# Performance work log

Hardware: AMD Instinct MI355X
Metric: run time of the kernel (lower is better)

The kernel has to match this reference:

```python
import jax, jax.numpy as jnp
import numpy as np

DIM = 1024
HEADS = 8
EV = DIM  # dim*expand - dim with expand=2
P = 2.0   # power-softmax exponent
EPS = 1e-5


def setup_inputs() -> dict:
    key = jax.random.key(0)
    k1, k2, k3 = jax.random.split(key, 3)
    B, L = 4, 2048
    x = jax.random.normal(k1, (B, L, DIM), dtype=jnp.float32)
    gamma = jnp.ones((DIM,), dtype=jnp.float32)
    beta = jnp.zeros((DIM,), dtype=jnp.float32)
    # torch nn.Linear weights are [out_features, in_features]
    w_qkv = jax.random.normal(k2, (5 * DIM, DIM), dtype=jnp.float32) * (DIM ** -0.5)
    w_out = jax.random.normal(k3, (DIM, 2 * DIM), dtype=jnp.float32) * ((2 * DIM) ** -0.5)
    return {"x": x, "gamma": gamma, "beta": beta, "w_qkv": w_qkv, "w_out": w_out}


def _layernorm(x, gamma, beta):
    xf = x.astype(jnp.float32)
    mu = jnp.mean(xf, axis=-1, keepdims=True)
    var = jnp.mean(jnp.square(xf - mu), axis=-1, keepdims=True)
    return ((xf - mu) * jax.lax.rsqrt(var + EPS)) * gamma + beta


def _p_softmax(scores, scale, p):
    # scores: [B,H,L,L] with -inf on masked entries
    s = scores.astype(jnp.float32) * scale
    if p == 1.0:
        return jax.nn.softmax(s, axis=-1)
    lse = jax.nn.logsumexp(s * p, axis=-1, keepdims=True) / p
    return jnp.exp(s - lse)


def _attention(q, k, v, heads, p):
    B, L, D = q.shape
    hd = D // heads
    q = q.reshape(B, L, heads, hd).transpose(0, 2, 1, 3)  # bhld
    k = k.reshape(B, L, heads, hd).transpose(0, 2, 1, 3)
    v = v.reshape(B, L, heads, hd).transpose(0, 2, 1, 3)
    scores = jnp.einsum('bhqd,bhkd->bhqk', q, k)
    mask = jnp.tril(jnp.ones((L, L), dtype=bool))
    scores = jnp.where(mask, scores, -jnp.inf)
    probs = _p_softmax(scores, hd ** -0.5, p).astype(q.dtype)
    out = jnp.einsum('bhqk,bhkd->bhqd', probs, v)
    return out.transpose(0, 2, 1, 3).reshape(B, L, D)


def reference(x, gamma, beta, w_qkv, w_out):
    h = _layernorm(x, gamma, beta).astype(x.dtype)
    proj = h @ w_qkv.T  # [B,L,5*DIM]
    q, k, v, lin, pre = jnp.split(proj, np.cumsum([DIM, DIM, DIM, EV]), axis=-1)
    attn = _attention(q, k, v, HEADS, P)
    branch = jnp.concatenate([lin * jax.nn.gelu(pre, approximate=False), attn], axis=-1)
    return x + branch @ w_out.T
```

## Files before the change

kernel.cpp:

```cpp
#include <hip/hip_runtime.h>
#include <hip/hip_bf16.h>
#include <math.h>

#define DIMD 1024
#define LSEQ 2048
#define BATCH 4
#define NHEAD 8
#define HD 128
#define NROWS (BATCH*LSEQ)
#define PROJC (5*DIMD)
#define BRC (2*DIMD)

typedef __attribute__((ext_vector_type(8))) short short8;
typedef __attribute__((ext_vector_type(4))) short short4v;
typedef __attribute__((ext_vector_type(4))) float floatx4;

__device__ __forceinline__ float bf2f(short s) {
  unsigned int u = ((unsigned int)(unsigned short)s) << 16;
  return __builtin_bit_cast(float, u);
}
__device__ __forceinline__ short f2bf(float f) {
  unsigned int u = __builtin_bit_cast(unsigned int, f);
  unsigned int lsb = (u >> 16) & 1u;
  u += 0x7fffu + lsb;
  return (short)(u >> 16);
}

__device__ __forceinline__ void gl2lds16(const short* g, short* l) {
  __builtin_amdgcn_global_load_lds(
      (const __attribute__((address_space(1))) unsigned int*)(unsigned long long)g,
      (__attribute__((address_space(3))) unsigned int*)(unsigned int)(unsigned long long)l,
      16, 0, 0);
}

__device__ __forceinline__ void wgbar() {
  asm volatile("" ::: "memory");
  __builtin_amdgcn_s_barrier();
  asm volatile("" ::: "memory");
}

__global__ __launch_bounds__(256) void cvt2_kernel(const float* __restrict__ s1,
    short* __restrict__ d1, int n1_4, const float* __restrict__ s2,
    short* __restrict__ d2, int n2_4) {
  int i = blockIdx.x * 256 + threadIdx.x;
  const float* src; short* dst;
  if (i < n1_4) { src = s1; dst = d1; }
  else { i -= n1_4; if (i >= n2_4) return; src = s2; dst = d2; }
  float4 v = *(const float4*)(src + (size_t)i * 4);
  short4v o;
  o[0] = f2bf(v.x); o[1] = f2bf(v.y); o[2] = f2bf(v.z); o[3] = f2bf(v.w);
  *(short4v*)(dst + (size_t)i * 4) = o;
}

__global__ __launch_bounds__(256) void ln_kernel(const float* __restrict__ x,
    const float* __restrict__ gamma, const float* __restrict__ beta,
    short* __restrict__ h) {
  int row = blockIdx.x;
  int c = threadIdx.x * 4;
  const float* xr = x + (size_t)row * DIMD;
  float4 v = *(const float4*)(xr + c);
  float f[4] = {v.x, v.y, v.z, v.w};
  float sum = 0.f, sq = 0.f;
  for (int i = 0; i < 4; ++i) { sum += f[i]; sq += f[i]*f[i]; }
  for (int off = 1; off < 64; off <<= 1) {
    sum += __shfl_xor(sum, off);
    sq  += __shfl_xor(sq, off);
  }
  __shared__ float red[8];
  int wid = threadIdx.x >> 6;
  if ((threadIdx.x & 63) == 0) { red[wid*2] = sum; red[wid*2+1] = sq; }
  __syncthreads();
  sum = red[0]+red[2]+red[4]+red[6];
  sq  = red[1]+red[3]+red[5]+red[7];
  float mu = sum * (1.0f/DIMD);
  float var = sq * (1.0f/DIMD) - mu*mu;
  float rstd = rsqrtf(var + 1e-5f);
  float4 g = *(const float4*)(gamma + c);
  float4 bb = *(const float4*)(beta + c);
  float gg[4] = {g.x, g.y, g.z, g.w};
  float bv[4] = {bb.x, bb.y, bb.z, bb.w};
  short4v o;
  for (int i = 0; i < 4; ++i)
    o[i] = f2bf((f[i] - mu) * rstd * gg[i] + bv[i]);
  *(short4v*)(h + (size_t)row * DIMD + c) = o;
}


__device__ __forceinline__ void rd_a(const short* base, int s0, int s1,
                                     short8 (&a)[4][2]) {
#pragma unroll
  for (int m = 0; m < 4; ++m) {
    a[m][0] = *(const short8*)(base + m*16*64 + s0);
    a[m][1] = *(const short8*)(base + m*16*64 + s1);
  }
}
__device__ __forceinline__ void rd_b(const short* base, int s0, int s1,
                                     short8 (&b)[2][2]) {
#pragma unroll
  for (int n = 0; n < 2; ++n) {
    b[n][0] = *(const short8*)(base + n*16*64 + s0);
    b[n][1] = *(const short8*)(base + n*16*64 + s1);
  }
}
template<int QM, int QN>
__device__ __forceinline__ void qmm(const short8 (&a)[4][2], const short8 (&b)[2][2],
                                    floatx4 (&acc)[8][4]) {
  __builtin_amdgcn_s_setprio(1);
#pragma unroll
  for (int m = 0; m < 4; ++m)
#pragma unroll
    for (int n = 0; n < 2; ++n) {
      floatx4 c = acc[QM*4+m][QN*2+n];
      c = __builtin_amdgcn_mfma_f32_16x16x32_bf16(a[m][0], b[n][0], c, 0, 0, 0);
      c = __builtin_amdgcn_mfma_f32_16x16x32_bf16(a[m][1], b[n][1], c, 0, 0, 0);
      acc[QM*4+m][QN*2+n] = c;
    }
  __builtin_amdgcn_s_setprio(0);
}
__device__ __forceinline__ void stg2(const short* p, int K, short* lds) {
  gl2lds16(p, lds);
  gl2lds16(p + (size_t)64*K, lds + 64*64);
}
__device__ __forceinline__ void stg4(const short* p, int K, short* lds, int koff) {
  stg2(p + koff, K, lds);
  stg2(p + (size_t)128*K + koff, K, lds + 128*64);
}

__global__ __launch_bounds__(512, 2) void gemm256(const short* __restrict__ A,
    const short* __restrict__ W, short* __restrict__ C, int M, int N, int K) {
  __shared__ __align__(16) short AsF[2*256*64];
  __shared__ __align__(16) short WsF[2*256*64];
  const int tid = threadIdx.x;
  const int lane = tid & 63, wv = tid >> 6;
  const int wm = wv >> 2, wn = wv & 3;
  const int quad = lane >> 4, l16 = lane & 15;

  const int nbx = N >> 8;
  int cpx = gridDim.x >> 3;
  int orig = blockIdx.x;
  int wg = (orig & 7) * cpx + (orig >> 3);
  int bx = wg % nbx, by = wg / nbx;
  const int row0 = by << 8, col0 = bx << 8;

  const int lrow = lane >> 3;
  const int sslot = (lane & 7) ^ lrow;
  const short* pA = A + (size_t)(row0 + wv*8 + lrow) * K + sslot*8;
  const short* pW = W + (size_t)(col0 + wv*8 + lrow) * K + sslot*8;
  short* stA = AsF + wv*8*64;
  short* stW = WsF + wv*8*64;
  const short* aB = AsF + (wm*128 + l16)*64;
  const short* wB = WsF + (wn*64 + l16)*64;
  const int s0 = (quad ^ (l16 & 7)) << 3;
  const int s1 = s0 ^ 32;

  floatx4 acc[8][4] = {};
  short8 a[4][2], b0[2][2], b1[2][2];

  const int nktm = (K >> 6) - 1;

  stg4(pA, K, stA, 0);
  stg4(pW, K, stW, 0);
  stg4(pA, K, stA + 16384, 64);
  asm volatile("s_waitcnt vmcnt(4)" ::: "memory");
  wgbar();

  const int NT = K >> 6;
  for (int t = 0; t < NT; ++t) {
    const int cur = (t & 1) << 14;
    const int nxt = cur ^ 16384;
    const int kw1 = ((t + 1) & nktm) << 6;
    const int ka2 = ((t + 2) & nktm) << 6;
    rd_a(aB + cur, s0, s1, a);
    rd_b(wB + cur, s0, s1, b0);
    stg4(pW, K, stW + nxt, kw1);
    wgbar();
    qmm<0,0>(a, b0, acc);
    rd_b(wB + cur + 32*64, s0, s1, b1);
    wgbar();
    qmm<0,1>(a, b1, acc);
    rd_a(aB + cur + 64*64, s0, s1, a);
    wgbar();
    qmm<1,1>(a, b1, acc);
    wgbar();
    stg4(pA, K, stA + cur, ka2);
    qmm<1,0>(a, b0, acc);
    asm volatile("s_waitcnt vmcnt(4)" ::: "memory");
    wgbar();
  }
  asm volatile("s_waitcnt vmcnt(0)" ::: "memory");

#pragma unroll
  for (int i = 0; i < 8; ++i) {
    int r0 = row0 + wm*128 + i*16 + quad*4;
#pragma unroll
    for (int j = 0; j < 4; ++j) {
      int cc = col0 + wn*64 + j*16 + l16;
#pragma unroll
      for (int r = 0; r < 4; ++r)
        C[(size_t)(r0 + r) * N + cc] = f2bf(acc[i][j][r]);
    }
  }
}

template<int MODE>
__global__ __launch_bounds__(256) void gemm_bt(const short* __restrict__ A,
    const short* __restrict__ W, const float* __restrict__ X,
    void* __restrict__ Cv, int M, int N, int K) {
  __shared__ __align__(16) short As[128*64];
  __shared__ __align__(16) short Ws[128*64];
  int tid = threadIdx.x;
  int row0 = blockIdx.y * 128;
  int col0 = blockIdx.x * 128;
  int lane = tid & 63, wv = tid >> 6;
  int wr = (wv >> 1) * 64, wc = (wv & 1) * 64;
  int quad = lane >> 4, l16 = lane & 15;
  floatx4 acc[4][4] = {};
  int srow = lane >> 3;
  int gq = ((lane & 7) - srow) & 7;
  const short* Ag = A + (size_t)(row0 + wv*8 + srow) * K + gq*8;
  const short* Wg = W + (size_t)(col0 + wv*8 + srow) * K + gq*8;
  short* Al = As + wv*8*64;
  short* Wl = Ws + wv*8*64;
  int qsr0 = (((quad)     + (l16 & 7)) & 7) * 8;
  int qsr1 = (((quad + 4) + (l16 & 7)) & 7) * 8;
  for (int k0 = 0; k0 < K; k0 += 64) {
    __syncthreads();
    for (int c = 0; c < 4; ++c) {
      gl2lds16(Ag + k0 + (size_t)(c*32)*K, Al + c*32*64);
      gl2lds16(Wg + k0 + (size_t)(c*32)*K, Wl + c*32*64);
    }
    __syncthreads();
    short8 af[4], wf[4];
    for (int i = 0; i < 4; ++i) af[i] = *(const short8*)&As[(wr + i*16 + l16)*64 + qsr0];
    for (int j = 0; j < 4; ++j) wf[j] = *(const short8*)&Ws[(wc + j*16 + l16)*64 + qsr0];
    for (int i = 0; i < 4; ++i)
      for (int j = 0; j < 4; ++j)
        acc[i][j] = __builtin_amdgcn_mfma_f32_16x16x32_bf16(af[i], wf[j], acc[i][j], 0, 0, 0);
    for (int i = 0; i < 4; ++i) af[i] = *(const short8*)&As[(wr + i*16 + l16)*64 + qsr1];
    for (int j = 0; j < 4; ++j) wf[j] = *(const short8*)&Ws[(wc + j*16 + l16)*64 + qsr1];
    for (int i = 0; i < 4; ++i)
      for (int j = 0; j < 4; ++j)
        acc[i][j] = __builtin_amdgcn_mfma_f32_16x16x32_bf16(af[i], wf[j], acc[i][j], 0, 0, 0);
  }
  for (int i = 0; i < 4; ++i) {
    int r0 = row0 + wr + i*16 + quad*4;
    for (int j = 0; j < 4; ++j) {
      int cc = col0 + wc + j*16 + l16;
      for (int r = 0; r < 4; ++r) {
        float v = acc[i][j][r];
        size_t idx = (size_t)(r0 + r) * N + cc;
        if (MODE == 0) {
          ((short*)Cv)[idx] = f2bf(v);
        } else {
          ((float*)Cv)[idx] = v + X[idx];
        }
      }
    }
  }
}

__global__ __launch_bounds__(256) void gelu_kernel(const short* __restrict__ proj,
    short* __restrict__ branch) {
  int row = blockIdx.x;
  int c = threadIdx.x * 4;
  const short* pr = proj + (size_t)row * PROJC;
  short4v lin = *(const short4v*)(pr + 3*DIMD + c);
  short4v pre = *(const short4v*)(pr + 4*DIMD + c);
  short4v o;
  for (int i = 0; i < 4; ++i) {
    float xx = bf2f(pre[i]);
    float g = 0.5f * xx * (1.f + erff(xx * 0.70710678118654752f));
    o[i] = f2bf(bf2f(lin[i]) * g);
  }
  *(short4v*)(branch + (size_t)row * BRC + c) = o;
}

__global__ __launch_bounds__(256) void vt_kernel(const short* __restrict__ proj,
    short* __restrict__ vt) {
  int bh = blockIdx.y;
  int b = bh >> 3, hh = bh & 7;
  int l0 = blockIdx.x * 64;
  __shared__ short Ls[64][136];
  int tid = threadIdx.x;
  int r = tid >> 4, c = (tid & 15) * 8;
  const short* Vp = proj + (size_t)b * LSEQ * PROJC + 2*DIMD + hh*HD;
  for (int p = 0; p < 4; ++p)
    *(short8*)&Ls[r + p*16][c] = *(const short8*)(Vp + (size_t)(l0 + r + p*16) * PROJC + c);
  __syncthreads();
  int d = tid >> 1, lh = (tid & 1) * 32;
  short* outp = vt + ((size_t)bh * HD + d) * LSEQ + l0 + lh;
  for (int g = 0; g < 4; ++g) {
    short8 o;
    for (int j = 0; j < 8; ++j) o[j] = Ls[lh + g*8 + j][d];
    *(short8*)(outp + g*8) = o;
  }
}

__global__ __launch_bounds__(512) void attn_kernel(const short* __restrict__ proj,
    const short* __restrict__ vt, short* __restrict__ branch) {
  int bh = blockIdx.y;
  int b = bh >> 3, hh = bh & 7;
  int gx = blockIdx.x;
  int gsel = (bh < 16) ? gx : (15 - gx);
  int tid = threadIdx.x;
  int wv = tid >> 6, lane = tid & 63, quad = lane >> 4, l16 = lane & 15;
  int qsel = 2*gsel + ((wv < 4) ? 0 : 1);
  int qw = qsel * 64 + (wv & 3) * 16;

  const short* Qp  = proj + (size_t)b * LSEQ * PROJC + hh*HD;
  const short* Kp  = Qp + DIMD;
  const short* VTp = vt + (size_t)bh * HD * LSEQ;

  __shared__ short Ks[64][136];
  __shared__ short Vs[128][76];
  __shared__ short Ps[8][16][44];

  short8 qf[4];
  {
    const short* qrow = Qp + (size_t)(qw + l16) * PROJC;
    for (int s = 0; s < 4; ++s) qf[s] = *(const short8*)(qrow + s*32 + quad*8);
  }
  float lsum[4] = {0.f, 0.f, 0.f, 0.f};
  floatx4 O[8] = {};

  const float scale = 0.08838834764831845f;
  int NT = 2*gsel + 2;
  int krow = tid >> 4;
  int kcol = (tid & 15) * 8;
  int vd = tid >> 2;
  int vk = (tid & 3) * 8;

  short8 kv0 = *(const short8*)(Kp + (size_t)(krow) * PROJC + kcol);
  short8 kv1 = *(const short8*)(Kp + (size_t)(32 + krow) * PROJC + kcol);
  short8 vv0 = *(const short8*)(VTp + (size_t)vd * LSEQ + vk);
  short8 vv1 = *(const short8*)(VTp + (size_t)vd * LSEQ + 32 + vk);

  for (int kt = 0; kt < NT; ++kt) {
    int kb64 = kt * 64;
    __syncthreads();
    *(short8*)&Ks[krow][kcol]      = kv0;
    *(short8*)&Ks[krow + 32][kcol] = kv1;
    *(short8*)&Vs[vd][vk]          = vv0;
    *(short8*)&Vs[vd][32 + vk]     = vv1;
    {
      int ktn = (kt + 1 < NT) ? (kt + 1) : kt;
      int kb64n = ktn * 64;
      kv0 = *(const short8*)(Kp + (size_t)(kb64n + krow) * PROJC + kcol);
      kv1 = *(const short8*)(Kp + (size_t)(kb64n + 32 + krow) * PROJC + kcol);
      vv0 = *(const short8*)(VTp + (size_t)vd * LSEQ + kb64n + vk);
      vv1 = *(const short8*)(VTp + (size_t)vd * LSEQ + kb64n + 32 + vk);
    }
    __syncthreads();
    for (int hf = 0; hf < 2; ++hf) {
      int kb = kb64 + hf*32;
      if (kb <= qw + 15) {
        floatx4 s0 = {0.f,0.f,0.f,0.f}, s1 = {0.f,0.f,0.f,0.f};
        for (int s = 0; s < 4; ++s) {
          short8 kf0 = *(const short8*)&Ks[hf*32 + l16][s*32 + quad*8];
          short8 kf1 = *(const short8*)&Ks[hf*32 + 16 + l16][s*32 + quad*8];
          s0 = __builtin_amdgcn_mfma_f32_16x16x32_bf16(qf[s], kf0, s0, 0, 0, 0);
          s1 = __builtin_amdgcn_mfma_f32_16x16x32_bf16(qf[s], kf1, s1, 0, 0, 0);
        }
        int c0 = kb + l16, c1 = kb + 16 + l16;
        for (int r = 0; r < 4; ++r) {
          int q = qw + quad*4 + r;
          float w0 = (c0 <= q) ? __expf(s0[r] * scale) : 0.f;
          float w1 = (c1 <= q) ? __expf(s1[r] * scale) : 0.f;
          lsum[r] += w0*w0 + w1*w1;
          Ps[wv][quad*4+r][l16]      = f2bf(w0);
          Ps[wv][quad*4+r][16 + l16] = f2bf(w1);
        }
        asm volatile("s_waitcnt lgkmcnt(0)" ::: "memory");
        short8 pf = *(const short8*)&Ps[wv][l16][quad*8];
        for (int t8 = 0; t8 < 8; ++t8) {
          short8 vf = *(const short8*)&Vs[t8*16 + l16][hf*32 + quad*8];
          O[t8] = __builtin_amdgcn_mfma_f32_16x16x32_bf16(pf, vf, O[t8], 0, 0, 0);
        }
      }
    }
  }
  for (int r = 0; r < 4; ++r) {
    float l = lsum[r];
    for (int off = 1; off < 16; off <<= 1) l += __shfl_xor(l, off);
    float inv = rsqrtf(l);
    int q = qw + quad*4 + r;
    short* orow = branch + ((size_t)(b*LSEQ + q)) * BRC + DIMD + hh*HD;
    for (int t8 = 0; t8 < 8; ++t8)
      orow[t8*16 + l16] = f2bf(O[t8][r] * inv);
  }
}

extern "C" void kernel_launch(void* const* d_in, const int* in_sizes, int n_in,
                              void* d_out, int out_size, void* d_ws, size_t ws_size,
                              hipStream_t stream) {
  const float* x     = (const float*)d_in[0];
  const float* gamma = (const float*)d_in[1];
  const float* beta  = (const float*)d_in[2];
  const float* w_qkv = (const float*)d_in[3];
  const float* w_out = (const float*)d_in[4];
  float* out = (float*)d_out;

  char* ws = (char*)d_ws;
  short* h      = (short*)ws;
  short* proj   = (short*)(ws + (size_t)16*1024*1024);
  short* branch = (short*)(ws + (size_t)96*1024*1024);
  short* wq     = (short*)(ws + (size_t)128*1024*1024);
  short* wo     = (short*)(ws + (size_t)138*1024*1024);
  short* vt     = h;

  int n1 = PROJC*DIMD/4, n2 = DIMD*BRC/4;
  cvt2_kernel<<<(n1 + n2 + 255)/256, 256, 0, stream>>>(w_qkv, wq, n1, w_out, wo, n2);
  ln_kernel<<<NROWS, 256, 0, stream>>>(x, gamma, beta, h);
  gemm256<<<dim3((NROWS/256)*(PROJC/256)), 512, 0, stream>>>(h, wq, proj,
                                                             NROWS, PROJC, DIMD);
  gelu_kernel<<<NROWS, 256, 0, stream>>>(proj, branch);
  vt_kernel<<<dim3(LSEQ/64, BATCH*NHEAD), 256, 0, stream>>>(proj, vt);
  attn_kernel<<<dim3(16, BATCH*NHEAD), 512, 0, stream>>>(proj, vt, branch);
  gemm_bt<1><<<dim3(DIMD/128, NROWS/128), 256, 0, stream>>>(branch, wo, x, out,
                                                            NROWS, DIMD, BRC);
}
```

Baseline: 350.9 us.

## Replace output GEMM with double-buffered 128x256 pipelined kernel and XCD-aware block remap

Replaces the simple single-buffered 128x128 output-projection GEMM with a 512-thread kernel that computes 128x256 tiles. It double-buffers A and W tiles in LDS, issues global-to-LDS loads for the next k-step while MFMAs run, and uses XOR-swizzled LDS slots. It also remaps block indices so neighbouring tiles land on the same XCD, which should improve L2 reuse. The aim is to hide load latency and cut barrier stalls in the final GEMM, at the cost of more LDS per block and a more complex schedule.

```diff
diff --git a/kernel.cpp b/kernel.cpp
--- a/kernel.cpp
+++ b/kernel.cpp
@@ -85,7 +85,6 @@
   *(short4v*)(h + (size_t)row * DIMD + c) = o;
 }
 
-
 __device__ __forceinline__ void rd_a(const short* base, int s0, int s1,
                                      short8 (&a)[4][2]) {
 #pragma unroll
@@ -114,6 +113,21 @@
       c = __builtin_amdgcn_mfma_f32_16x16x32_bf16(a[m][0], b[n][0], c, 0, 0, 0);
       c = __builtin_amdgcn_mfma_f32_16x16x32_bf16(a[m][1], b[n][1], c, 0, 0, 0);
       acc[QM*4+m][QN*2+n] = c;
+    }
+  __builtin_amdgcn_s_setprio(0);
+}
+template<int QN>
+__device__ __forceinline__ void qmm2(const short8 (&a)[4][2], const short8 (&b)[2][2],
+                                     floatx4 (&acc)[4][4]) {
+  __builtin_amdgcn_s_setprio(1);
+#pragma unroll
+  for (int m = 0; m < 4; ++m)
+#pragma unroll
+    for (int n = 0; n < 2; ++n) {
+      floatx4 c = acc[m][QN*2+n];
+      c = __builtin_amdgcn_mfma_f32_16x16x32_bf16(a[m][0], b[n][0], c, 0, 0, 0);
+      c = __builtin_amdgcn_mfma_f32_16x16x32_bf16(a[m][1], b[n][1], c, 0, 0, 0);
+      acc[m][QN*2+n] = c;
     }
   __builtin_amdgcn_s_setprio(0);
 }
@@ -202,58 +216,76 @@
   }
 }
 
-template<int MODE>
-__global__ __launch_bounds__(256) void gemm_bt(const short* __restrict__ A,
+__global__ __launch_bounds__(512, 2) void gemm2(const short* __restrict__ A,
     const short* __restrict__ W, const float* __restrict__ X,
-    void* __restrict__ Cv, int M, int N, int K) {
-  __shared__ __align__(16) short As[128*64];
-  __shared__ __align__(16) short Ws[128*64];
-  int tid = threadIdx.x;
-  int row0 = blockIdx.y * 128;
-  int col0 = blockIdx.x * 128;
-  int lane = tid & 63, wv = tid >> 6;
-  int wr = (wv >> 1) * 64, wc = (wv & 1) * 64;
-  int quad = lane >> 4, l16 = lane & 15;
+    float* __restrict__ out, int M, int N, int K) {
+  __shared__ __align__(16) short As2[2*128*64];
+  __shared__ __align__(16) short Ws2[2*256*64];
+  const int tid = threadIdx.x;
+  const int lane = tid & 63, wv = tid >> 6;
+  const int wm = wv >> 2, wn = wv & 3;
+  const int quad = lane >> 4, l16 = lane & 15;
+
+  const int nbx = N >> 8;
+  int cpx = gridDim.x >> 3;
+  int orig = blockIdx.x;
+  int wg = (orig & 7) * cpx + (orig >> 3);
+  int bx = wg % nbx, by = wg / nbx;
+  const int row0 = by << 7, col0 = bx << 8;
+
+  const int lrow = lane >> 3;
+  const int sslot = (lane & 7) ^ lrow;
+  const short* pA = A + (size_t)(row0 + wv*8 + lrow) * K + sslot*8;
+  const short* pW = W + (size_t)(col0 + wv*8 + lrow) * K + sslot*8;
+  short* stA = As2 + wv*8*64;
+  short* stW = Ws2 + wv*8*64;
+  const short* aB = As2 + (wm*64 + l16)*64;
+  const short* wB = Ws2 + (wn*64 + l16)*64;
+  const int s0 = (quad ^ (l16 & 7)) << 3;
+  const int s1 = s0 ^ 32;
+
   floatx4 acc[4][4] = {};
-  int srow = lane >> 3;
-  int gq = ((lane & 7) - srow) & 7;
-  const short* Ag = A + (size_t)(row0 + wv*8 + srow) * K + gq*8;
-  const short* Wg = W + (size_t)(col0 + wv*8 + srow) * K + gq*8;
-  short* Al = As + wv*8*64;
-  short* Wl = Ws + wv*8*64;
-  int qsr0 = (((quad)     + (l16 & 7)) & 7) * 8;
-  int qsr1 = (((quad + 4) + (l16 & 7)) & 7) * 8;
-  for (int k0 = 0; k0 < K; k0 += 64) {
-    __syncthreads();
-    for (int c = 0; c < 4; ++c) {
-      gl2lds16(Ag + k0 + (size_t)(c*32)*K, Al + c*32*64);
-      gl2lds16(Wg + k0 + (size_t)(c*32)*K, Wl + c*32*64);
-    }
-    __syncthreads();
-    short8 af[4], wf[4];
-    for (int i = 0; i < 4; ++i) af[i] = *(const short8*)&As[(wr + i*16 + l16)*64 + qsr0];
-    for (int j = 0; j < 4; ++j) wf[j] = *(const short8*)&Ws[(wc + j*16 + l16)*64 + qsr0];
-    for (int i = 0; i < 4; ++i)
-      for (int j = 0; j < 4; ++j)
-        acc[i][j] = __builtin_amdgcn_mfma_f32_16x16x32_bf16(af[i], wf[j], acc[i][j], 0, 0, 0);
-    for (int i = 0; i < 4; ++i) af[i] = *(const short8*)&As[(wr + i*16 + l16)*64 + qsr1];
-    for (int j = 0; j < 4; ++j) wf[j] = *(const short8*)&Ws[(wc + j*16 + l16)*64 + qsr1];
-    for (int i = 0; i < 4; ++i)
-      for (int j = 0; j < 4; ++j)
-        acc[i][j] = __builtin_amdgcn_mfma_f32_16x16x32_bf16(af[i], wf[j], acc[i][j], 0, 0, 0);
-  }
+  short8 a[4][2], b0[2][2], b1[2][2];
+
+  const int nktm = (K >> 6) - 1;
+
+  stg2(pA, K, stA);
+  stg4(pW, K, stW, 0);
+  stg2(pA + 64, K, stA + 8192);
+  asm volatile("s_waitcnt vmcnt(2)" ::: "memory");
+  wgbar();
+
+  const int NT = K >> 6;
+  for (int t = 0; t < NT; ++t) {
+    const int curA = (t & 1) << 13;
+    const int curW = (t & 1) << 14;
+    const int nxtW = curW ^ 16384;
+    const int kw1 = ((t + 1) & nktm) << 6;
+    const int ka2 = ((t + 2) & nktm) << 6;
+    rd_a(aB + curA, s0, s1, a);
+    rd_b(wB + curW, s0, s1, b0);
+    stg4(pW, K, stW + nxtW, kw1);
+    wgbar();
+    qmm2<0>(a, b0, acc);
+    rd_b(wB + curW + 32*64, s0, s1, b1);
+    wgbar();
+    stg2(pA + ka2, K, stA + curA);
+    qmm2<1>(a, b1, acc);
+    asm volatile("s_waitcnt vmcnt(2)" ::: "memory");
+    wgbar();
+  }
+  asm volatile("s_waitcnt vmcnt(0)" ::: "memory");
+
+#pragma unroll
   for (int i = 0; i < 4; ++i) {
-    int r0 = row0 + wr + i*16 + quad*4;
+    int r0 = row0 + wm*64 + i*16 + quad*4;
+#pragma unroll
     for (int j = 0; j < 4; ++j) {
-      int cc = col0 + wc + j*16 + l16;
+      int cc = col0 + wn*64 + j*16 + l16;
+#pragma unroll
       for (int r = 0; r < 4; ++r) {
-        float v = acc[i][j][r];
         size_t idx = (size_t)(r0 + r) * N + cc;
-        if (MODE == 0) {
-          ((short*)Cv)[idx] = f2bf(v);
-        } else {
-          ((float*)Cv)[idx] = v + X[idx];
-        }
+        out[idx] = acc[i][j][r] + X[idx];
       }
     }
   }
@@ -416,6 +448,5 @@
   gelu_kernel<<<NROWS, 256, 0, stream>>>(proj, branch);
   vt_kernel<<<dim3(LSEQ/64, BATCH*NHEAD), 256, 0, stream>>>(proj, vt);
   attn_kernel<<<dim3(16, BATCH*NHEAD), 512, 0, stream>>>(proj, vt, branch);
-  gemm_bt<1><<<dim3(DIMD/128, NROWS/128), 256, 0, stream>>>(branch, wo, x, out,
-                                                            NROWS, DIMD, BRC);
-}
+  gemm2<<<dim3(256), 512, 0, stream>>>(branch, wo, x, out, NROWS, DIMD, BRC);
+}
```

After: 322.4 us. -8.1%, faster.
